# Performance work log

Measured on AMD Instinct MI355X. Metric: run time of the kernel, lower is better.

The kernel has to match this reference:

```python
import jax, jax.numpy as jnp
import numpy as np

N_NODES = 50000
N_EDGES = 800000
D_IN, D_HID, D_OUT = 64, 128, 64


def _glorot(key, fan_in, fan_out):
    lim = (6.0 / (fan_in + fan_out)) ** 0.5
    return jax.random.uniform(key, (fan_in, fan_out), jnp.float32, -lim, lim)


def setup_inputs() -> dict:
    key = jax.random.key(0)
    ks = jax.random.split(key, 10)
    x = jax.random.normal(ks[0], (N_NODES, D_IN), jnp.float32)
    edge_index = jax.random.randint(ks[1], (2, N_EDGES), 0, N_NODES, jnp.int64)
    # GINConv1 MLP: Linear(D_IN->D_HID), ReLU, Linear(D_HID->D_HID)
    W1a = _glorot(ks[2], D_IN, D_HID); b1a = jnp.zeros((D_HID,), jnp.float32)
    W1b = _glorot(ks[3], D_HID, D_HID); b1b = jnp.zeros((D_HID,), jnp.float32)
    # GINConv2 MLP: Linear(D_HID->D_HID), ReLU, Linear(D_HID->D_OUT)
    W2a = _glorot(ks[4], D_HID, D_HID); b2a = jnp.zeros((D_HID,), jnp.float32)
    W2b = _glorot(ks[5], D_HID, D_OUT); b2b = jnp.zeros((D_OUT,), jnp.float32)
    return {"x": x, "edge_index": edge_index,
            "W1a": W1a, "b1a": b1a, "W1b": W1b, "b1b": b1b,
            "W2a": W2a, "b2a": b2a, "W2b": W2b, "b2b": b2b}


def _gin_conv(x, src, dst, Wa, ba, Wb, bb):
    # GIN aggregation (eps = 0): h_i = x_i + sum_{j in N(i)} x_j
    msgs = x[src]                                   # [E, d] gather
    agg = jax.ops.segment_sum(msgs, dst, num_segments=x.shape[0])  # [N, d]
    h = x + agg
    # 2-layer MLP
    h = jax.nn.relu(h @ Wa + ba)
    return h @ Wb + bb


def reference(x, edge_index, W1a, b1a, W1b, b1b, W2a, b2a, W2b, b2b):
    src, dst = edge_index[0], edge_index[1]
    h = jax.nn.relu(_gin_conv(x, src, dst, W1a, b1a, W1b, b1b))
    h = jax.nn.relu(_gin_conv(h, src, dst, W2a, b2a, W2b, b2b))
    return h
```

## Files before the change

### kernel.cpp

```cpp
#include <hip/hip_runtime.h>

#define N_NODES 50000
#define N_EDGES 800000

typedef __attribute__((ext_vector_type(8))) short short8;
typedef __attribute__((ext_vector_type(4))) float floatx4;

static __device__ __forceinline__ unsigned short f2b(float f) {
    unsigned int u = __float_as_uint(f);
    unsigned int r = u + 0x7fffu + ((u >> 16) & 1u);
    return (unsigned short)(r >> 16);
}
static __device__ __forceinline__ unsigned int pk(float a, float b) {
    return (unsigned)f2b(a) | ((unsigned)f2b(b) << 16);
}
static __device__ __forceinline__ float blo(unsigned int u) {
    return __uint_as_float(u << 16);
}
static __device__ __forceinline__ float bhi(unsigned int u) {
    return __uint_as_float(u & 0xffff0000u);
}

__global__ void hist_rank_kernel(const int* __restrict__ dst,
                                 int* __restrict__ deg, int* __restrict__ rank,
                                 int n) {
    int i = blockIdx.x * blockDim.x + threadIdx.x;
    if (i < n) rank[i] = atomicAdd(&deg[dst[i]], 1);
}

__global__ __launch_bounds__(1024) void scanA_kernel(
    const int* __restrict__ deg, int* __restrict__ bsum, int n) {
    __shared__ int s[1024];
    const int tid = threadIdx.x;
    int i = blockIdx.x * 1024 + tid;
    s[tid] = (i < n) ? deg[i] : 0;
    __syncthreads();
    for (int d = 512; d > 0; d >>= 1) {
        if (tid < d) s[tid] += s[tid + d];
        __syncthreads();
    }
    if (tid == 0) bsum[blockIdx.x] = s[0];
}

__global__ __launch_bounds__(1024) void scanC_kernel(
    const int* __restrict__ deg, const int* __restrict__ bsum,
    int* __restrict__ off, int n) {
    __shared__ int s[1024];
    __shared__ int bpref;
    const int tid = threadIdx.x;
    if (tid == 0) {
        int p = 0;
        for (int j = 0; j < blockIdx.x; ++j) p += bsum[j];
        bpref = p;
    }
    const int i = blockIdx.x * 1024 + tid;
    const int v = (i < n) ? deg[i] : 0;
    s[tid] = v;
    __syncthreads();
    for (int d = 1; d < 1024; d <<= 1) {
        int t = (tid >= d) ? s[tid - d] : 0;
        __syncthreads();
        s[tid] += t;
        __syncthreads();
    }
    const int excl = s[tid] - v + bpref;
    if (i < n) {
        off[i] = excl;
        if (i == n - 1) off[n] = excl + v;
    }
}

__global__ void fill_kernel(const int* __restrict__ src,
                            const int* __restrict__ dst,
                            const int* __restrict__ rank,
                            const int* __restrict__ off,
                            unsigned short* __restrict__ nbr, int n) {
    int i = blockIdx.x * blockDim.x + threadIdx.x;
    if (i < n) nbr[off[dst[i]] + rank[i]] = (unsigned short)src[i];
}

__global__ __launch_bounds__(256) void prep_kernel(
    const float* __restrict__ W1a, const float* __restrict__ W1b,
    const float* __restrict__ W2a, const float* __restrict__ W2b,
    const float* __restrict__ x, unsigned short* __restrict__ W1aT,
    unsigned short* __restrict__ W1bT, unsigned short* __restrict__ W2aT,
    unsigned short* __restrict__ W2bT, unsigned short* __restrict__ xb,
    int* __restrict__ deg) {
    int i = blockIdx.x * 256 + threadIdx.x;
    if (i < 8192) {
        int n = i >> 6, k = i & 63;
        W1aT[i] = f2b(W1a[k * 128 + n]);
    } else if (i < 24576) {
        int j = i - 8192, n = j >> 7, k = j & 127;
        W1bT[j] = f2b(W1b[k * 128 + n]);
    } else if (i < 40960) {
        int j = i - 24576, n = j >> 7, k = j & 127;
        W2aT[j] = f2b(W2a[k * 128 + n]);
    } else if (i < 49152) {
        int j = i - 40960, n = j >> 7, k = j & 127;
        W2bT[j] = f2b(W2b[k * 64 + n]);
    } else if (i < 49152 + N_NODES * 16) {
        int j = i - 49152;
        float4 v = ((const float4*)x)[j];
        uint2 o;
        o.x = pk(v.x, v.y);
        o.y = pk(v.z, v.w);
        ((uint2*)xb)[j] = o;
    } else {
        int j = i - (49152 + N_NODES * 16);
        if (j < N_NODES) deg[j] = 0;
    }
}

template <int DIN, int DH, int DOUT, bool OUT_BF16>
__global__ __launch_bounds__(256) void gin_fused_kernel(
    const unsigned short* __restrict__ xin, const int* __restrict__ off,
    const unsigned short* __restrict__ nbr,
    const unsigned short* __restrict__ WaT, const float* __restrict__ ba,
    const unsigned short* __restrict__ WbT, const float* __restrict__ bb,
    void* __restrict__ outp, int n_rows) {
    constexpr int ROWS = 32;
    constexpr int SA = DIN + 16;
    constexpr int SH = DH + 16;
    __shared__ __attribute__((aligned(16))) unsigned short tA[ROWS * SA];
    __shared__ __attribute__((aligned(16))) unsigned short hidA[ROWS * SH];

    const int tid = threadIdx.x;
    const int row0 = blockIdx.x * ROWS;
    const int grp = tid >> 4;
    const int c = tid & 15;

    for (int t = 0; t < 2; ++t) {
        const int r = grp * 2 + t;
        const int node = row0 + r;
        if (DIN == 64) {
            float f0 = 0.f, f1 = 0.f, f2 = 0.f, f3 = 0.f;
            if (node < n_rows) {
                const uint2* xr = (const uint2*)xin;
                const uint2 a = xr[(size_t)node * 16 + c];
                f0 = blo(a.x); f1 = bhi(a.x); f2 = blo(a.y); f3 = bhi(a.y);
                const int lo = off[node], hi = off[node + 1];
                int j = lo;
                for (; j + 4 <= hi; j += 4) {
                    const int s0 = nbr[j], s1 = nbr[j + 1], s2 = nbr[j + 2],
                              s3 = nbr[j + 3];
                    const uint2 v0 = xr[(size_t)s0 * 16 + c];
                    const uint2 v1 = xr[(size_t)s1 * 16 + c];
                    const uint2 v2 = xr[(size_t)s2 * 16 + c];
                    const uint2 v3 = xr[(size_t)s3 * 16 + c];
                    f0 += (blo(v0.x) + blo(v1.x)) + (blo(v2.x) + blo(v3.x));
                    f1 += (bhi(v0.x) + bhi(v1.x)) + (bhi(v2.x) + bhi(v3.x));
                    f2 += (blo(v0.y) + blo(v1.y)) + (blo(v2.y) + blo(v3.y));
                    f3 += (bhi(v0.y) + bhi(v1.y)) + (bhi(v2.y) + bhi(v3.y));
                }
                for (; j < hi; ++j) {
                    const uint2 v = xr[(size_t)nbr[j] * 16 + c];
                    f0 += blo(v.x); f1 += bhi(v.x);
                    f2 += blo(v.y); f3 += bhi(v.y);
                }
            }
            uint2 o;
            o.x = pk(f0, f1);
            o.y = pk(f2, f3);
            *(uint2*)&tA[r * SA + c * 4] = o;
        } else {
            float f0 = 0.f, f1 = 0.f, f2 = 0.f, f3 = 0.f;
            float f4 = 0.f, f5 = 0.f, f6 = 0.f, f7 = 0.f;
            if (node < n_rows) {
                const uint4* hr = (const uint4*)xin;
                const uint4 a = hr[(size_t)node * 16 + c];
                f0 = blo(a.x); f1 = bhi(a.x); f2 = blo(a.y); f3 = bhi(a.y);
                f4 = blo(a.z); f5 = bhi(a.z); f6 = blo(a.w); f7 = bhi(a.w);
                const int lo = off[node], hi = off[node + 1];
                int j = lo;
                for (; j + 4 <= hi; j += 4) {
                    const int s0 = nbr[j], s1 = nbr[j + 1], s2 = nbr[j + 2],
                              s3 = nbr[j + 3];
                    const uint4 v0 = hr[(size_t)s0 * 16 + c];
                    const uint4 v1 = hr[(size_t)s1 * 16 + c];
                    const uint4 v2 = hr[(size_t)s2 * 16 + c];
                    const uint4 v3 = hr[(size_t)s3 * 16 + c];
                    f0 += (blo(v0.x) + blo(v1.x)) + (blo(v2.x) + blo(v3.x));
                    f1 += (bhi(v0.x) + bhi(v1.x)) + (bhi(v2.x) + bhi(v3.x));
                    f2 += (blo(v0.y) + blo(v1.y)) + (blo(v2.y) + blo(v3.y));
                    f3 += (bhi(v0.y) + bhi(v1.y)) + (bhi(v2.y) + bhi(v3.y));
                    f4 += (blo(v0.z) + blo(v1.z)) + (blo(v2.z) + blo(v3.z));
                    f5 += (bhi(v0.z) + bhi(v1.z)) + (bhi(v2.z) + bhi(v3.z));
                    f6 += (blo(v0.w) + blo(v1.w)) + (blo(v2.w) + blo(v3.w));
                    f7 += (bhi(v0.w) + bhi(v1.w)) + (bhi(v2.w) + bhi(v3.w));
                }
                for (; j < hi; ++j) {
                    const uint4 v = hr[(size_t)nbr[j] * 16 + c];
                    f0 += blo(v.x); f1 += bhi(v.x);
                    f2 += blo(v.y); f3 += bhi(v.y);
                    f4 += blo(v.z); f5 += bhi(v.z);
                    f6 += blo(v.w); f7 += bhi(v.w);
                }
            }
            uint4 o;
            o.x = pk(f0, f1); o.y = pk(f2, f3);
            o.z = pk(f4, f5); o.w = pk(f6, f7);
            *(uint4*)&tA[r * SA + c * 8] = o;
        }
    }
    __syncthreads();

    const int lane = tid & 63;
    const int wv = tid >> 6;
    const int wm = wv & 1;
    const int wn = wv >> 1;
    const int quad = lane >> 4;
    const int l16 = lane & 15;
    const int m0 = wm * 16;

    short8 a1[DIN / 32];
#pragma unroll
    for (int kk = 0; kk < DIN / 32; ++kk)
        a1[kk] = *(const short8*)&tA[(m0 + l16) * SA + kk * 32 + quad * 8];
#pragma unroll
    for (int nt = 0; nt < DH / 32; ++nt) {
        const int col = wn * (DH / 2) + nt * 16 + l16;
        floatx4 acc = {0.f, 0.f, 0.f, 0.f};
#pragma unroll
        for (int kk = 0; kk < DIN / 32; ++kk) {
            short8 b = *(const short8*)&WaT[col * DIN + kk * 32 + quad * 8];
            acc = __builtin_amdgcn_mfma_f32_16x16x32_bf16(a1[kk], b, acc, 0, 0, 0);
        }
        const float bias = ba[col];
#pragma unroll
        for (int r = 0; r < 4; ++r) {
            const float v = fmaxf(acc[r] + bias, 0.f);
            hidA[(m0 + quad * 4 + r) * SH + col] = f2b(v);
        }
    }
    __syncthreads();

    short8 a2[DH / 32];
#pragma unroll
    for (int kk = 0; kk < DH / 32; ++kk)
        a2[kk] = *(const short8*)&hidA[(m0 + l16) * SH + kk * 32 + quad * 8];
#pragma unroll
    for (int nt = 0; nt < DOUT / 32; ++nt) {
        const int col = wn * (DOUT / 2) + nt * 16 + l16;
        floatx4 acc = {0.f, 0.f, 0.f, 0.f};
#pragma unroll
        for (int kk = 0; kk < DH / 32; ++kk) {
            short8 b = *(const short8*)&WbT[col * DH + kk * 32 + quad * 8];
            acc = __builtin_amdgcn_mfma_f32_16x16x32_bf16(a2[kk], b, acc, 0, 0, 0);
        }
        const float bias = bb[col];
#pragma unroll
        for (int r = 0; r < 4; ++r) {
            const float v = fmaxf(acc[r] + bias, 0.f);
            const int grow = row0 + m0 + quad * 4 + r;
            if (grow < n_rows) {
                if (OUT_BF16)
                    ((unsigned short*)outp)[(size_t)grow * DOUT + col] = f2b(v);
                else
                    ((float*)outp)[(size_t)grow * DOUT + col] = v;
            }
        }
    }
}

extern "C" void kernel_launch(void* const* d_in, const int* in_sizes, int n_in,
                              void* d_out, int out_size, void* d_ws,
                              size_t ws_size, hipStream_t stream) {
    const float* x   = (const float*)d_in[0];
    const int*   ei  = (const int*)d_in[1];
    const float* W1a = (const float*)d_in[2];
    const float* b1a = (const float*)d_in[3];
    const float* W1b = (const float*)d_in[4];
    const float* b1b = (const float*)d_in[5];
    const float* W2a = (const float*)d_in[6];
    const float* b2a = (const float*)d_in[7];
    const float* W2b = (const float*)d_in[8];
    const float* b2b = (const float*)d_in[9];
    float* out = (float*)d_out;

    const int* src = ei;
    const int* dst = ei + N_EDGES;

    unsigned short* xb = (unsigned short*)d_ws;
    unsigned short* h  = xb + (size_t)N_NODES * 64;
    unsigned short* W1aT = h + (size_t)N_NODES * 128;
    unsigned short* W1bT = W1aT + 8192;
    unsigned short* W2aT = W1bT + 16384;
    unsigned short* W2bT = W2aT + 16384;
    int* deg  = (int*)(W2bT + 8192);
    int* off  = deg + N_NODES;
    int* bsum = off + N_NODES + 1;
    int* rank = bsum + 64;
    unsigned short* nbr = (unsigned short*)(rank + N_EDGES);

    constexpr int NB = (N_NODES + 1023) / 1024;
    constexpr int PREP_THREADS = 49152 + N_NODES * 16 + N_NODES;

    prep_kernel<<<(PREP_THREADS + 255) / 256, 256, 0, stream>>>(
        W1a, W1b, W2a, W2b, x, W1aT, W1bT, W2aT, W2bT, xb, deg);

    hist_rank_kernel<<<(N_EDGES + 255) / 256, 256, 0, stream>>>(dst, deg, rank,
                                                                N_EDGES);
    scanA_kernel<<<NB, 1024, 0, stream>>>(deg, bsum, N_NODES);
    scanC_kernel<<<NB, 1024, 0, stream>>>(deg, bsum, off, N_NODES);
    fill_kernel<<<(N_EDGES + 255) / 256, 256, 0, stream>>>(src, dst, rank, off,
                                                           nbr, N_EDGES);

    gin_fused_kernel<64, 128, 128, true>
        <<<(N_NODES + 31) / 32, 256, 0, stream>>>(xb, off, nbr, W1aT, b1a, W1bT,
                                                  b1b, h, N_NODES);

    gin_fused_kernel<128, 128, 64, false>
        <<<(N_NODES + 31) / 32, 256, 0, stream>>>(h, off, nbr, W2aT, b2a, W2bT,
                                                  b2b, out, N_NODES);
}
```

Before: 232.6 us.

## Pad CSR neighbor lists to multiples of four with a zero sentinel row

Each node's neighbor list is padded to a multiple of four using a sentinel index that points at a zeroed extra row in the bf16 feature buffers. The aggregation loop can then read indices in vectorized groups with no scalar tail. Gathers switch to 16-byte loads with a thread-per-row mapping that adapts to the input width, so layer 2 uses 16-row blocks and twice as many blocks. The cost is extra padded gathers of the zero row and a larger nbr array. The fill kernel also gets extra threads to write the padding.

```diff
diff --git a/kernel.cpp b/kernel.cpp
--- a/kernel.cpp
+++ b/kernel.cpp
@@ -19,6 +19,18 @@
 }
 static __device__ __forceinline__ float bhi(unsigned int u) {
     return __uint_as_float(u & 0xffff0000u);
+}
+
+static __device__ __forceinline__ void acc4(float* f, uint4 v0, uint4 v1,
+                                            uint4 v2, uint4 v3) {
+    f[0] += (blo(v0.x) + blo(v1.x)) + (blo(v2.x) + blo(v3.x));
+    f[1] += (bhi(v0.x) + bhi(v1.x)) + (bhi(v2.x) + bhi(v3.x));
+    f[2] += (blo(v0.y) + blo(v1.y)) + (blo(v2.y) + blo(v3.y));
+    f[3] += (bhi(v0.y) + bhi(v1.y)) + (bhi(v2.y) + bhi(v3.y));
+    f[4] += (blo(v0.z) + blo(v1.z)) + (blo(v2.z) + blo(v3.z));
+    f[5] += (bhi(v0.z) + bhi(v1.z)) + (bhi(v2.z) + bhi(v3.z));
+    f[6] += (blo(v0.w) + blo(v1.w)) + (blo(v2.w) + blo(v3.w));
+    f[7] += (bhi(v0.w) + bhi(v1.w)) + (bhi(v2.w) + bhi(v3.w));
 }
 
 __global__ void hist_rank_kernel(const int* __restrict__ dst,
@@ -33,7 +45,7 @@
     __shared__ int s[1024];
     const int tid = threadIdx.x;
     int i = blockIdx.x * 1024 + tid;
-    s[tid] = (i < n) ? deg[i] : 0;
+    s[tid] = (i < n) ? ((deg[i] + 3) & ~3) : 0;
     __syncthreads();
     for (int d = 512; d > 0; d >>= 1) {
         if (tid < d) s[tid] += s[tid + d];
@@ -54,7 +66,7 @@
         bpref = p;
     }
     const int i = blockIdx.x * 1024 + tid;
-    const int v = (i < n) ? deg[i] : 0;
+    const int v = (i < n) ? ((deg[i] + 3) & ~3) : 0;
     s[tid] = v;
     __syncthreads();
     for (int d = 1; d < 1024; d <<= 1) {
@@ -74,9 +86,19 @@
                             const int* __restrict__ dst,
                             const int* __restrict__ rank,
                             const int* __restrict__ off,
-                            unsigned short* __restrict__ nbr, int n) {
+                            const int* __restrict__ deg,
+                            unsigned short* __restrict__ nbr, int n,
+                            int n_nodes) {
     int i = blockIdx.x * blockDim.x + threadIdx.x;
-    if (i < n) nbr[off[dst[i]] + rank[i]] = (unsigned short)src[i];
+    if (i < n) {
+        nbr[off[dst[i]] + rank[i]] = (unsigned short)src[i];
+    } else if (i < n + n_nodes) {
+        const int v = i - n;
+        const int base = off[v];
+        const int d = deg[v];
+        const int pd = (d + 3) & ~3;
+        for (int k = d; k < pd; ++k) nbr[base + k] = (unsigned short)N_NODES;
+    }
 }
 
 __global__ __launch_bounds__(256) void prep_kernel(
@@ -85,7 +107,7 @@
     const float* __restrict__ x, unsigned short* __restrict__ W1aT,
     unsigned short* __restrict__ W1bT, unsigned short* __restrict__ W2aT,
     unsigned short* __restrict__ W2bT, unsigned short* __restrict__ xb,
-    int* __restrict__ deg) {
+    unsigned short* __restrict__ h, int* __restrict__ deg) {
     int i = blockIdx.x * 256 + threadIdx.x;
     if (i < 8192) {
         int n = i >> 6, k = i & 63;
@@ -106,9 +128,16 @@
         o.x = pk(v.x, v.y);
         o.y = pk(v.z, v.w);
         ((uint2*)xb)[j] = o;
+    } else if (i < 49152 + N_NODES * 16 + N_NODES) {
+        int j = i - (49152 + N_NODES * 16);
+        deg[j] = 0;
     } else {
-        int j = i - (49152 + N_NODES * 16);
-        if (j < N_NODES) deg[j] = 0;
+        int j = i - (49152 + N_NODES * 16 + N_NODES);
+        uint4 z = {0u, 0u, 0u, 0u};
+        if (j < 8)
+            ((uint4*)(xb + (size_t)N_NODES * 64))[j] = z;
+        else if (j < 24)
+            ((uint4*)(h + (size_t)N_NODES * 128))[j - 8] = z;
     }
 }
 
@@ -119,7 +148,8 @@
     const unsigned short* __restrict__ WaT, const float* __restrict__ ba,
     const unsigned short* __restrict__ WbT, const float* __restrict__ bb,
     void* __restrict__ outp, int n_rows) {
-    constexpr int ROWS = 32;
+    constexpr int LPR = DIN / 8;
+    constexpr int ROWS = 256 / LPR;
     constexpr int SA = DIN + 16;
     constexpr int SH = DH + 16;
     __shared__ __attribute__((aligned(16))) unsigned short tA[ROWS * SA];
@@ -127,88 +157,63 @@
 
     const int tid = threadIdx.x;
     const int row0 = blockIdx.x * ROWS;
-    const int grp = tid >> 4;
-    const int c = tid & 15;
-
-    for (int t = 0; t < 2; ++t) {
-        const int r = grp * 2 + t;
-        const int node = row0 + r;
-        if (DIN == 64) {
-            float f0 = 0.f, f1 = 0.f, f2 = 0.f, f3 = 0.f;
-            if (node < n_rows) {
-                const uint2* xr = (const uint2*)xin;
-                const uint2 a = xr[(size_t)node * 16 + c];
-                f0 = blo(a.x); f1 = bhi(a.x); f2 = blo(a.y); f3 = bhi(a.y);
-                const int lo = off[node], hi = off[node + 1];
-                int j = lo;
-                for (; j + 4 <= hi; j += 4) {
-                    const int s0 = nbr[j], s1 = nbr[j + 1], s2 = nbr[j + 2],
-                              s3 = nbr[j + 3];
-                    const uint2 v0 = xr[(size_t)s0 * 16 + c];
-                    const uint2 v1 = xr[(size_t)s1 * 16 + c];
-                    const uint2 v2 = xr[(size_t)s2 * 16 + c];
-                    const uint2 v3 = xr[(size_t)s3 * 16 + c];
-                    f0 += (blo(v0.x) + blo(v1.x)) + (blo(v2.x) + blo(v3.x));
-                    f1 += (bhi(v0.x) + bhi(v1.x)) + (bhi(v2.x) + bhi(v3.x));
-                    f2 += (blo(v0.y) + blo(v1.y)) + (blo(v2.y) + blo(v3.y));
-                    f3 += (bhi(v0.y) + bhi(v1.y)) + (bhi(v2.y) + bhi(v3.y));
-                }
-                for (; j < hi; ++j) {
-                    const uint2 v = xr[(size_t)nbr[j] * 16 + c];
-                    f0 += blo(v.x); f1 += bhi(v.x);
-                    f2 += blo(v.y); f3 += bhi(v.y);
-                }
-            }
-            uint2 o;
-            o.x = pk(f0, f1);
-            o.y = pk(f2, f3);
-            *(uint2*)&tA[r * SA + c * 4] = o;
-        } else {
-            float f0 = 0.f, f1 = 0.f, f2 = 0.f, f3 = 0.f;
-            float f4 = 0.f, f5 = 0.f, f6 = 0.f, f7 = 0.f;
-            if (node < n_rows) {
-                const uint4* hr = (const uint4*)xin;
-                const uint4 a = hr[(size_t)node * 16 + c];
-                f0 = blo(a.x); f1 = bhi(a.x); f2 = blo(a.y); f3 = bhi(a.y);
-                f4 = blo(a.z); f5 = bhi(a.z); f6 = blo(a.w); f7 = bhi(a.w);
-                const int lo = off[node], hi = off[node + 1];
-                int j = lo;
-                for (; j + 4 <= hi; j += 4) {
-                    const int s0 = nbr[j], s1 = nbr[j + 1], s2 = nbr[j + 2],
-                              s3 = nbr[j + 3];
-                    const uint4 v0 = hr[(size_t)s0 * 16 + c];
-                    const uint4 v1 = hr[(size_t)s1 * 16 + c];
-                    const uint4 v2 = hr[(size_t)s2 * 16 + c];
-                    const uint4 v3 = hr[(size_t)s3 * 16 + c];
-                    f0 += (blo(v0.x) + blo(v1.x)) + (blo(v2.x) + blo(v3.x));
-                    f1 += (bhi(v0.x) + bhi(v1.x)) + (bhi(v2.x) + bhi(v3.x));
-                    f2 += (blo(v0.y) + blo(v1.y)) + (blo(v2.y) + blo(v3.y));
-                    f3 += (bhi(v0.y) + bhi(v1.y)) + (bhi(v2.y) + bhi(v3.y));
-                    f4 += (blo(v0.z) + blo(v1.z)) + (blo(v2.z) + blo(v3.z));
-                    f5 += (bhi(v0.z) + bhi(v1.z)) + (bhi(v2.z) + bhi(v3.z));
-                    f6 += (blo(v0.w) + blo(v1.w)) + (blo(v2.w) + blo(v3.w));
-                    f7 += (bhi(v0.w) + bhi(v1.w)) + (bhi(v2.w) + bhi(v3.w));
-                }
-                for (; j < hi; ++j) {
-                    const uint4 v = hr[(size_t)nbr[j] * 16 + c];
-                    f0 += blo(v.x); f1 += bhi(v.x);
-                    f2 += blo(v.y); f3 += bhi(v.y);
-                    f4 += blo(v.z); f5 += bhi(v.z);
-                    f6 += blo(v.w); f7 += bhi(v.w);
-                }
-            }
-            uint4 o;
-            o.x = pk(f0, f1); o.y = pk(f2, f3);
-            o.z = pk(f4, f5); o.w = pk(f6, f7);
-            *(uint4*)&tA[r * SA + c * 8] = o;
-        }
-    }
+    const int grp = tid / LPR;
+    const int c = tid % LPR;
+    const int node = row0 + grp;
+
+    float f[8] = {0.f, 0.f, 0.f, 0.f, 0.f, 0.f, 0.f, 0.f};
+    const uint4* xr = (const uint4*)xin;
+    if (node < n_rows) {
+        const uint4 a = xr[(size_t)node * LPR + c];
+        f[0] = blo(a.x); f[1] = bhi(a.x);
+        f[2] = blo(a.y); f[3] = bhi(a.y);
+        f[4] = blo(a.z); f[5] = bhi(a.z);
+        f[6] = blo(a.w); f[7] = bhi(a.w);
+        const int lo = off[node], hi = off[node + 1];
+        int j = lo;
+        for (; j + 8 <= hi; j += 8) {
+            const uint2 i0 = *(const uint2*)&nbr[j];
+            const uint2 i1 = *(const uint2*)&nbr[j + 4];
+            const int s0 = i0.x & 0xffff, s1 = i0.x >> 16;
+            const int s2 = i0.y & 0xffff, s3 = i0.y >> 16;
+            const int s4 = i1.x & 0xffff, s5 = i1.x >> 16;
+            const int s6 = i1.y & 0xffff, s7 = i1.y >> 16;
+            const uint4 v0 = xr[(size_t)s0 * LPR + c];
+            const uint4 v1 = xr[(size_t)s1 * LPR + c];
+            const uint4 v2 = xr[(size_t)s2 * LPR + c];
+            const uint4 v3 = xr[(size_t)s3 * LPR + c];
+            const uint4 v4 = xr[(size_t)s4 * LPR + c];
+            const uint4 v5 = xr[(size_t)s5 * LPR + c];
+            const uint4 v6 = xr[(size_t)s6 * LPR + c];
+            const uint4 v7 = xr[(size_t)s7 * LPR + c];
+            acc4(f, v0, v1, v2, v3);
+            acc4(f, v4, v5, v6, v7);
+        }
+        if (j < hi) {
+            const uint2 i0 = *(const uint2*)&nbr[j];
+            const int s0 = i0.x & 0xffff, s1 = i0.x >> 16;
+            const int s2 = i0.y & 0xffff, s3 = i0.y >> 16;
+            const uint4 v0 = xr[(size_t)s0 * LPR + c];
+            const uint4 v1 = xr[(size_t)s1 * LPR + c];
+            const uint4 v2 = xr[(size_t)s2 * LPR + c];
+            const uint4 v3 = xr[(size_t)s3 * LPR + c];
+            acc4(f, v0, v1, v2, v3);
+        }
+    }
+    uint4 o;
+    o.x = pk(f[0], f[1]);
+    o.y = pk(f[2], f[3]);
+    o.z = pk(f[4], f[5]);
+    o.w = pk(f[6], f[7]);
+    *(uint4*)&tA[grp * SA + c * 8] = o;
     __syncthreads();
 
+    constexpr int MT = ROWS / 16;
+    constexpr int NSPLIT = 4 / MT;
     const int lane = tid & 63;
     const int wv = tid >> 6;
-    const int wm = wv & 1;
-    const int wn = wv >> 1;
+    const int wm = wv % MT;
+    const int wn = wv / MT;
     const int quad = lane >> 4;
     const int l16 = lane & 15;
     const int m0 = wm * 16;
@@ -218,8 +223,8 @@
     for (int kk = 0; kk < DIN / 32; ++kk)
         a1[kk] = *(const short8*)&tA[(m0 + l16) * SA + kk * 32 + quad * 8];
 #pragma unroll
-    for (int nt = 0; nt < DH / 32; ++nt) {
-        const int col = wn * (DH / 2) + nt * 16 + l16;
+    for (int nt = 0; nt < DH / (16 * NSPLIT); ++nt) {
+        const int col = wn * (DH / NSPLIT) + nt * 16 + l16;
         floatx4 acc = {0.f, 0.f, 0.f, 0.f};
 #pragma unroll
         for (int kk = 0; kk < DIN / 32; ++kk) {
@@ -240,8 +245,8 @@
     for (int kk = 0; kk < DH / 32; ++kk)
         a2[kk] = *(const short8*)&hidA[(m0 + l16) * SH + kk * 32 + quad * 8];
 #pragma unroll
-    for (int nt = 0; nt < DOUT / 32; ++nt) {
-        const int col = wn * (DOUT / 2) + nt * 16 + l16;
+    for (int nt = 0; nt < DOUT / (16 * NSPLIT); ++nt) {
+        const int col = wn * (DOUT / NSPLIT) + nt * 16 + l16;
         floatx4 acc = {0.f, 0.f, 0.f, 0.f};
 #pragma unroll
         for (int kk = 0; kk < DH / 32; ++kk) {
@@ -282,8 +287,8 @@
     const int* dst = ei + N_EDGES;
 
     unsigned short* xb = (unsigned short*)d_ws;
-    unsigned short* h  = xb + (size_t)N_NODES * 64;
-    unsigned short* W1aT = h + (size_t)N_NODES * 128;
+    unsigned short* h  = xb + (size_t)(N_NODES + 1) * 64;
+    unsigned short* W1aT = h + (size_t)(N_NODES + 1) * 128;
     unsigned short* W1bT = W1aT + 8192;
     unsigned short* W2aT = W1bT + 16384;
     unsigned short* W2bT = W2aT + 16384;
@@ -294,23 +299,23 @@
     unsigned short* nbr = (unsigned short*)(rank + N_EDGES);
 
     constexpr int NB = (N_NODES + 1023) / 1024;
-    constexpr int PREP_THREADS = 49152 + N_NODES * 16 + N_NODES;
+    constexpr int PREP_THREADS = 49152 + N_NODES * 16 + N_NODES + 24;
 
     prep_kernel<<<(PREP_THREADS + 255) / 256, 256, 0, stream>>>(
-        W1a, W1b, W2a, W2b, x, W1aT, W1bT, W2aT, W2bT, xb, deg);
+        W1a, W1b, W2a, W2b, x, W1aT, W1bT, W2aT, W2bT, xb, h, deg);
 
     hist_rank_kernel<<<(N_EDGES + 255) / 256, 256, 0, stream>>>(dst, deg, rank,
                                                                 N_EDGES);
     scanA_kernel<<<NB, 1024, 0, stream>>>(deg, bsum, N_NODES);
     scanC_kernel<<<NB, 1024, 0, stream>>>(deg, bsum, off, N_NODES);
-    fill_kernel<<<(N_EDGES + 255) / 256, 256, 0, stream>>>(src, dst, rank, off,
-                                                           nbr, N_EDGES);
+    fill_kernel<<<(N_EDGES + N_NODES + 255) / 256, 256, 0, stream>>>(
+        src, dst, rank, off, deg, nbr, N_EDGES, N_NODES);
 
     gin_fused_kernel<64, 128, 128, true>
         <<<(N_NODES + 31) / 32, 256, 0, stream>>>(xb, off, nbr, W1aT, b1a, W1bT,
                                                   b1b, h, N_NODES);
 
     gin_fused_kernel<128, 128, 64, false>
-        <<<(N_NODES + 31) / 32, 256, 0, stream>>>(h, off, nbr, W2aT, b2a, W2bT,
+        <<<(N_NODES + 15) / 16, 256, 0, stream>>>(h, off, nbr, W2aT, b2a, W2bT,
                                                   b2b, out, N_NODES);
 }
```

New measurement: 218.3 us. -6.2%, faster.
